# Kernel optimization log

Measured on AMD Instinct MI355X. Metric: run time of the kernel, lower is better.

Reference implementation:

```python
import jax, jax.numpy as jnp
import numpy as np
from jax import lax

STRIDE = 2
PADDING = 2
KERNEL = 5


def _conv_transpose3d(x, weight, bias):
    # weight: [C_in, C_out, kd, kh, kw] (PyTorch ConvTranspose3d layout)
    # Equivalent dense conv: flip kernel spatially, swap in/out channels,
    # lhs_dilation=stride, symmetric padding = dilation*(k-1) - padding.
    w_t = jnp.flip(weight, axis=(2, 3, 4)).transpose(1, 0, 2, 3, 4)  # [C_out, C_in, k,k,k]
    pad = KERNEL - 1 - PADDING  # = 2
    y = lax.conv_general_dilated(
        x, w_t,
        window_strides=(1, 1, 1),
        padding=[(pad, pad)] * 3,
        lhs_dilation=(STRIDE, STRIDE, STRIDE),
        dimension_numbers=("NCDHW", "OIDHW", "NCDHW"),
    )
    return y + bias[None, :, None, None, None]


def _maxpool3d(y, k):
    # PyTorch MaxPool3d(kernel=k) -> stride=k, no padding, floor mode == VALID
    win = (1, 1, k, k, k)
    return lax.reduce_window(y, -jnp.inf, lax.max, win, win, "VALID")


def setup_inputs() -> dict:
    key = jax.random.key(0)
    k1, k2, k3 = jax.random.split(key, 3)
    x = jax.random.normal(k1, (16, 32, 16, 32, 32), dtype=jnp.float32)
    weight = jax.random.normal(k2, (32, 64, 5, 5, 5), dtype=jnp.float32) * 0.05
    bias = jax.random.normal(k3, (64,), dtype=jnp.float32) * 0.05
    return {"x": x, "weight": weight, "bias": bias}


def reference(x, weight, bias):
    y = _conv_transpose3d(x, weight, bias)     # [16, 64, 31, 63, 63]
    y = _maxpool3d(y, 2)                       # [16, 64, 15, 31, 31]
    y = _maxpool3d(y, 3)                       # [16, 64, 5, 10, 10]
    return jnp.sum(y, axis=1, keepdims=True)   # [16, 1, 5, 10, 10]
```

## Files before the change

kernel.cpp:

```cpp
#include <hip/hip_runtime.h>
#include <hip/hip_bf16.h>
#include <math.h>

typedef short bf16x8 __attribute__((ext_vector_type(8)));
typedef float f32x4 __attribute__((ext_vector_type(4)));

constexpr int CIN = 32, COUT = 64, D = 16, H = 32, W = 32;

constexpr size_t WS_NEED = 884736u;

static __device__ const unsigned char IT_CODE[24] = {
    0, 8, 16, 3,
    1, 9, 17, 11, 19, 7,
    2, 10, 18, 5, 13, 21, 15,
    4, 12, 20, 6, 14, 22, 23};
static __device__ const unsigned char IT_START[5] = {0, 4, 10, 17, 24};
static __device__ const unsigned char EPI_START[10] = {0, 1, 3, 5, 6, 7, 9, 11, 12, 13};
static __device__ const unsigned char EPI_CNT[10]   = {1, 2, 2, 1, 1, 2, 2, 1, 1, 2};

__global__ void prep_w(const float* __restrict__ w, unsigned short* __restrict__ wtp) {
    int idx = blockIdx.x * 256 + threadIdx.x;
    int ci  = idx & 31;
    int co  = (idx >> 5) & 63;
    int tt  = idx >> 11;
    int t   = tt % 27, cls = tt / 27;
    int td = t / 9, th = (t / 3) % 3, tw = t % 3;
    int pd = (cls >> 2) & 1, ph = (cls >> 1) & 1, pw = cls & 1;
    int kd = pd + 2 * td, kh = ph + 2 * th, kw = pw + 2 * tw;
    float v = 0.f;
    if (kd < 5 && kh < 5 && kw < 5)
        v = w[(ci * COUT + co) * 125 + kd * 25 + kh * 5 + kw];
    __hip_bfloat16 b = __float2bfloat16(v);
    wtp[idx] = *reinterpret_cast<unsigned short*>(&b);
}

__device__ __forceinline__ int lpA(int wrow, int quad) {
    return wrow * 64 + ((quad ^ ((wrow >> 1) & 3)) << 4);
}

#define MFMA_G(nt, bb)                                                                       \
    acc[0][0][nt] = __builtin_amdgcn_mfma_f32_16x16x32_bf16(a##bb##0, b##bb##nt, acc[0][0][nt], 0, 0, 0); \
    acc[0][1][nt] = __builtin_amdgcn_mfma_f32_16x16x32_bf16(a##bb##1, b##bb##nt, acc[0][1][nt], 0, 0, 0); \
    acc[1][0][nt] = __builtin_amdgcn_mfma_f32_16x16x32_bf16(a##bb##2, b##bb##nt, acc[1][0][nt], 0, 0, 0); \
    acc[1][1][nt] = __builtin_amdgcn_mfma_f32_16x16x32_bf16(a##bb##3, b##bb##nt, acc[1][1][nt], 0, 0, 0); \
    acc[2][0][nt] = __builtin_amdgcn_mfma_f32_16x16x32_bf16(a##bb##4, b##bb##nt, acc[2][0][nt], 0, 0, 0); \
    acc[2][1][nt] = __builtin_amdgcn_mfma_f32_16x16x32_bf16(a##bb##5, b##bb##nt, acc[2][1][nt], 0, 0, 0);

#define LOADTAP(S)                                                                   \
    {                                                                                \
        int Boff = __builtin_amdgcn_readfirstlane((ptd * 9 + pth * 3 + ptw) * 4096); \
        int Qb   = __builtin_amdgcn_readfirstlane(((alpha + 2 - ptd) * 5 + (2 - pth)) * 2048); \
        int ss   = __builtin_amdgcn_readfirstlane(2 - ptw);                          \
        b##S##0 = *(const bf16x8*)(tbb + Boff);                                      \
        b##S##1 = *(const bf16x8*)(tbb + Boff + 1024);                               \
        b##S##2 = *(const bf16x8*)(tbb + Boff + 2048);                               \
        b##S##3 = *(const bf16x8*)(tbb + Boff + 3072);                               \
        int lpa = ss == 0 ? lp00 : (ss == 1 ? lp01 : lp02);                          \
        int lpb = ss == 0 ? lp10 : (ss == 1 ? lp11 : lp12);                          \
        const char* rb = xsb + Qb;                                                   \
        a##S##0 = *(const bf16x8*)(rb + lpa);                                        \
        a##S##1 = *(const bf16x8*)(rb + lpb);                                        \
        a##S##2 = *(const bf16x8*)(rb + 2048 + lpa);                                 \
        a##S##3 = *(const bf16x8*)(rb + 2048 + lpb);                                 \
        a##S##4 = *(const bf16x8*)(rb + 4096 + lpa);                                 \
        a##S##5 = *(const bf16x8*)(rb + 4096 + lpb);                                 \
    }

__global__ __launch_bounds__(256, 2) void main_k(
    const unsigned short* __restrict__ wtp, const float* __restrict__ x,
    const float* __restrict__ bias, float* __restrict__ out)
{
    __shared__ unsigned short Xs[25600];
    int bx = blockIdx.x;
    int h0 = bx % 10;
    int d0 = (bx / 10) % 5;
    int n  = bx / 50;
    int tid = threadIdx.x;

    int id0 = 3 * d0 - 1, ih0 = 3 * h0 - 1;
#pragma unroll 5
    for (int u = tid; u < 6400; u += 256) {
        int q  = u & 7;
        int ci = (u >> 3) & 31;
        int p  = u >> 8;
        int dd = p / 5, hl = p % 5;
        int id = id0 + dd, ih = ih0 + hl;
        float4 v = {0.f, 0.f, 0.f, 0.f};
        if (id >= 0 && ih >= 0)
            v = ((const float4*)(x + (((size_t)(n * CIN + ci) * D + id) * H + ih) * W))[q];
        unsigned short hj[4];
        {
            __hip_bfloat16 b0 = __float2bfloat16(v.x); hj[0] = *reinterpret_cast<unsigned short*>(&b0);
            __hip_bfloat16 b1 = __float2bfloat16(v.y); hj[1] = *reinterpret_cast<unsigned short*>(&b1);
            __hip_bfloat16 b2 = __float2bfloat16(v.z); hj[2] = *reinterpret_cast<unsigned short*>(&b2);
            __hip_bfloat16 b3 = __float2bfloat16(v.w); hj[3] = *reinterpret_cast<unsigned short*>(&b3);
        }
        int rowb = p * 1024;
        int cig = ci >> 3, cil = ci & 7;
#pragma unroll
        for (int j = 0; j < 4; ++j) {
            int ww = 4 * q + 1 + j;
            if (ww < 32)
                Xs[rowb + ww * 32 + ((cig ^ ((ww >> 1) & 3)) << 3) + cil] = hj[j];
        }
        if (q == 0)
            Xs[rowb + (cig << 3) + cil] = 0;
    }

    int lane = tid & 63, wv = tid >> 6;
    int l15 = lane & 15, quad = lane >> 4;
    int wv_s = __builtin_amdgcn_readfirstlane(wv);

    int laneB = l15 * 64 + quad * 16;
    int m1 = 16 + l15; if (m1 > 29) m1 = 29;
    int lp00 = lpA(l15 + 0, quad), lp01 = lpA(l15 + 1, quad), lp02 = lpA(l15 + 2, quad);
    int lp10 = lpA(m1 + 0, quad),  lp11 = lpA(m1 + 1, quad),  lp12 = lpA(m1 + 2, quad);

    int fsm0 = (0x3123 >> (quad * 4)) & 15;
    int fsm1 = (0x4312 >> (quad * 4)) & 15;

    float mxp[2][4][2];
#pragma unroll
    for (int mt = 0; mt < 2; ++mt)
#pragma unroll
        for (int nt = 0; nt < 4; ++nt) { mxp[mt][nt][0] = -INFINITY; mxp[mt][nt][1] = -INFINITY; }

    __syncthreads();
    const char* xsb = (const char*)Xs;

    int it0 = IT_START[wv_s], it1 = IT_START[wv_s + 1];
#pragma unroll 1
    for (int ii = it0; ii < it1; ++ii) {
        int code  = __builtin_amdgcn_readfirstlane(IT_CODE[ii]);
        int cls   = code & 7;
        int alpha = code >> 3;
        int ntd = 3 - ((cls >> 2) & 1), nth = 3 - ((cls >> 1) & 1), ntw = 3 - (cls & 1);
        const char* tbb = (const char*)wtp + (size_t)cls * 27 * 4096 + laneB;
        const int T = ntd * nth * ntw;

        f32x4 acc[3][2][4];
#pragma unroll
        for (int b = 0; b < 3; ++b)
#pragma unroll
            for (int mt = 0; mt < 2; ++mt)
#pragma unroll
                for (int nt = 0; nt < 4; ++nt) acc[b][mt][nt] = (f32x4){0.f, 0.f, 0.f, 0.f};

        int ptd = 0, pth = 0, ptw = 0, tl = 0;
        auto adv = [&]() {
            if (tl + 1 < T) {
                ++tl; ++ptw;
                if (ptw == ntw) { ptw = 0; ++pth; if (pth == nth) { pth = 0; ++ptd; } }
            }
        };

        bf16x8 bE0, bE1, bE2, bE3, aE0, aE1, aE2, aE3, aE4, aE5;
        bf16x8 bO0, bO1, bO2, bO3, aO0, aO1, aO2, aO3, aO4, aO5;
        LOADTAP(E) adv();
        LOADTAP(O) adv();

#pragma unroll 1
        for (int t = 0; t + 1 < T; t += 2) {
            __builtin_amdgcn_s_setprio(1);
            MFMA_G(0, E) MFMA_G(1, E) MFMA_G(2, E) MFMA_G(3, E)
            __builtin_amdgcn_s_setprio(0);
            LOADTAP(E) adv();
            __builtin_amdgcn_s_setprio(1);
            MFMA_G(0, O) MFMA_G(1, O) MFMA_G(2, O) MFMA_G(3, O)
            __builtin_amdgcn_s_setprio(0);
            LOADTAP(O) adv();
        }
        if (T & 1) {
            __builtin_amdgcn_s_setprio(1);
            MFMA_G(0, E) MFMA_G(1, E) MFMA_G(2, E) MFMA_G(3, E)
            __builtin_amdgcn_s_setprio(0);
        }

#pragma unroll
        for (int mt = 0; mt < 2; ++mt) {
            int fs = mt ? fsm1 : fsm0;
#pragma unroll
            for (int nt = 0; nt < 4; ++nt) {
                float r0 = fmaxf(fmaxf(acc[0][mt][nt][0], acc[1][mt][nt][0]), acc[2][mt][nt][0]);
                float r1 = fmaxf(fmaxf(acc[0][mt][nt][1], acc[1][mt][nt][1]), acc[2][mt][nt][1]);
                float r2 = fmaxf(fmaxf(acc[0][mt][nt][2], acc[1][mt][nt][2]), acc[2][mt][nt][2]);
                float r3 = fmaxf(fmaxf(acc[0][mt][nt][3], acc[1][mt][nt][3]), acc[2][mt][nt][3]);
                float t01 = fmaxf(r0, r1), t012 = fmaxf(t01, r2), t0123 = fmaxf(t012, r3);
                float pA = fs == 1 ? r0 : (fs == 2 ? t01 : (fs == 3 ? t012 : t0123));
                float t23 = fmaxf(r2, r3), t123 = fmaxf(r1, t23);
                float pB = fs == 1 ? t123 : (fs == 2 ? t23 : (fs == 3 ? r3 : -INFINITY));
                mxp[mt][nt][0] = fmaxf(mxp[mt][nt][0], pA);
                mxp[mt][nt][1] = fmaxf(mxp[mt][nt][1], pB);
            }
        }
    }

    __syncthreads();
    float* epi = (float*)Xs;
#pragma unroll
    for (int mt = 0; mt < 2; ++mt) {
        int g = mt * 4 + quad;
#pragma unroll
        for (int nt = 0; nt < 4; ++nt) {
            epi[((wv * 8 + g) * 2 + 0) * 64 + nt * 16 + l15] = mxp[mt][nt][0];
            epi[((wv * 8 + g) * 2 + 1) * 64 + nt * 16 + l15] = mxp[mt][nt][1];
        }
    }
    __syncthreads();

    int elemBase = ((n * 5 + d0) * 10 + h0) * 10;
    float bco = bias[lane];
#pragma unroll 1
    for (int win = wv_s; win < 10; win += 4) {
        int st = EPI_START[win], cnt = EPI_CNT[win];
        float v = -INFINITY;
        for (int src = 0; src < 4; ++src)
            for (int e = st; e < st + cnt; ++e)
                v = fmaxf(v, epi[(src * 16 + e) * 64 + lane]);
        v += bco;
#pragma unroll
        for (int off = 32; off > 0; off >>= 1) v += __shfl_xor(v, off);
        if (lane == 0) out[elemBase + win] = v;
    }
}

__global__ __launch_bounds__(256) void fused_fallback(
    const float* __restrict__ x, const float* __restrict__ wsrc,
    const float* __restrict__ bias, float* __restrict__ out)
{
    __shared__ float xs[CIN * 125];
    __shared__ float wmax[4][64];
    const int b  = blockIdx.x;
    const int w0 = b % 10, h0 = (b / 10) % 10, d0 = (b / 100) % 5, n = b / 500;
    const int tid = threadIdx.x;
    const int id0 = 3 * d0 - 1, ih0 = 3 * h0 - 1, iw0 = 3 * w0 - 1;
    for (int e = tid; e < CIN * 125; e += 256) {
        int kk = e % 5, jj = (e / 5) % 5, ii = (e / 25) % 5, c = e / 125;
        int id = id0 + ii, ih = ih0 + jj, iw = iw0 + kk;
        float v = 0.f;
        if (id >= 0 && ih >= 0 && iw >= 0)
            v = x[(((n * CIN + c) * D + id) * H + ih) * W + iw];
        xs[e] = v;
    }
    __syncthreads();
    const int lane = tid & 63, wv = tid >> 6;
    float lmax = -INFINITY;
    for (int ccls = 0; ccls < 2; ++ccls) {
        const int cls = wv * 2 + ccls;
        const int pd = (cls >> 2) & 1, ph = (cls >> 1) & 1, pw = cls & 1;
        float acc[27];
#pragma unroll
        for (int i = 0; i < 27; ++i) acc[i] = 0.f;
        for (int ci = 0; ci < CIN; ++ci) {
            float wr[27];
#pragma unroll
            for (int t = 0; t < 27; ++t) {
                int td = t / 9, th = (t / 3) % 3, tw = t % 3;
                int kd = pd + 2 * td, kh = ph + 2 * th, kw = pw + 2 * tw;
                wr[t] = (kd < 5 && kh < 5 && kw < 5)
                          ? wsrc[((ci * 64 + lane) * 125) + kd * 25 + kh * 5 + kw] : 0.f;
            }
            const float* xb = xs + ci * 125;
#pragma unroll
            for (int td = 0; td < 3; ++td)
#pragma unroll
            for (int th = 0; th < 3; ++th)
#pragma unroll
            for (int tw = 0; tw < 3; ++tw) {
                const float wval = wr[(td * 3 + th) * 3 + tw];
#pragma unroll
                for (int a = 0; a < 3; ++a)
#pragma unroll
                for (int bb = 0; bb < 3; ++bb)
#pragma unroll
                for (int cc = 0; cc < 3; ++cc)
                    acc[(a * 3 + bb) * 3 + cc] +=
                        xb[(a + 2 - td) * 25 + (bb + 2 - th) * 5 + (cc + 2 - tw)] * wval;
            }
        }
#pragma unroll
        for (int i = 0; i < 27; ++i) lmax = fmaxf(lmax, acc[i]);
    }
    wmax[wv][lane] = lmax;
    __syncthreads();
    if (wv == 0) {
        float m = fmaxf(fmaxf(wmax[0][lane], wmax[1][lane]),
                        fmaxf(wmax[2][lane], wmax[3][lane]));
        m += bias[lane];
        for (int off = 32; off > 0; off >>= 1) m += __shfl_down(m, off);
        if (lane == 0) out[b] = m;
    }
}

extern "C" void kernel_launch(void* const* d_in, const int* in_sizes, int n_in,
                              void* d_out, int out_size, void* d_ws, size_t ws_size,
                              hipStream_t stream) {
    const float* x    = (const float*)d_in[0];
    const float* w    = (const float*)d_in[1];
    const float* bias = (const float*)d_in[2];
    float* out = (float*)d_out;

    if (ws_size >= WS_NEED) {
        unsigned short* wtp = (unsigned short*)d_ws;
        prep_w<<<1728, 256, 0, stream>>>(w, wtp);
        main_k<<<800, 256, 0, stream>>>(wtp, x, bias, out);
    } else {
        fused_fallback<<<8000, 256, 0, stream>>>(x, w, bias, out);
    }
}
```

Baseline: 205.2 us.

## Switch main conv GEMM from 16x16x32 to 32x32x16 MFMA tiles

Replaces the 16x16x32 bf16 MFMA tiling with 32x32x16 MFMA, so each wave accumulates six 32x32 output tiles per tap. A and B operand addressing and the pooling fold are rewritten to match the new accumulator lane layout, and the epilogue scatters partial maxima into per-window LDS slots that are reduced with a fixed 8-way max. The aim is fewer MFMA instructions and LDS operand loads per FLOP, at the cost of more accumulator registers and a different epilogue shape. The tap loop also drops the clamped advance and guards the prefetches directly.

```diff
diff --git a/kernel.cpp b/kernel.cpp
--- a/kernel.cpp
+++ b/kernel.cpp
@@ -3,7 +3,7 @@
 #include <math.h>
 
 typedef short bf16x8 __attribute__((ext_vector_type(8)));
-typedef float f32x4 __attribute__((ext_vector_type(4)));
+typedef float f32x16 __attribute__((ext_vector_type(16)));
 
 constexpr int CIN = 32, COUT = 64, D = 16, H = 32, W = 32;
 
@@ -15,8 +15,6 @@
     2, 10, 18, 5, 13, 21, 15,
     4, 12, 20, 6, 14, 22, 23};
 static __device__ const unsigned char IT_START[5] = {0, 4, 10, 17, 24};
-static __device__ const unsigned char EPI_START[10] = {0, 1, 3, 5, 6, 7, 9, 11, 12, 13};
-static __device__ const unsigned char EPI_CNT[10]   = {1, 2, 2, 1, 1, 2, 2, 1, 1, 2};
 
 __global__ void prep_w(const float* __restrict__ w, unsigned short* __restrict__ wtp) {
     int idx = blockIdx.x * 256 + threadIdx.x;
@@ -34,36 +32,70 @@
     wtp[idx] = *reinterpret_cast<unsigned short*>(&b);
 }
 
-__device__ __forceinline__ int lpA(int wrow, int quad) {
-    return wrow * 64 + ((quad ^ ((wrow >> 1) & 3)) << 4);
-}
-
-#define MFMA_G(nt, bb)                                                                       \
-    acc[0][0][nt] = __builtin_amdgcn_mfma_f32_16x16x32_bf16(a##bb##0, b##bb##nt, acc[0][0][nt], 0, 0, 0); \
-    acc[0][1][nt] = __builtin_amdgcn_mfma_f32_16x16x32_bf16(a##bb##1, b##bb##nt, acc[0][1][nt], 0, 0, 0); \
-    acc[1][0][nt] = __builtin_amdgcn_mfma_f32_16x16x32_bf16(a##bb##2, b##bb##nt, acc[1][0][nt], 0, 0, 0); \
-    acc[1][1][nt] = __builtin_amdgcn_mfma_f32_16x16x32_bf16(a##bb##3, b##bb##nt, acc[1][1][nt], 0, 0, 0); \
-    acc[2][0][nt] = __builtin_amdgcn_mfma_f32_16x16x32_bf16(a##bb##4, b##bb##nt, acc[2][0][nt], 0, 0, 0); \
-    acc[2][1][nt] = __builtin_amdgcn_mfma_f32_16x16x32_bf16(a##bb##5, b##bb##nt, acc[2][1][nt], 0, 0, 0);
+__device__ __forceinline__ int lpA32(int row, int g) {
+    return row * 64 + ((g ^ ((row >> 1) & 3)) << 4);
+}
+
+#define RFL(x) __builtin_amdgcn_readfirstlane(x)
 
 #define LOADTAP(S)                                                                   \
     {                                                                                \
-        int Boff = __builtin_amdgcn_readfirstlane((ptd * 9 + pth * 3 + ptw) * 4096); \
-        int Qb   = __builtin_amdgcn_readfirstlane(((alpha + 2 - ptd) * 5 + (2 - pth)) * 2048); \
-        int ss   = __builtin_amdgcn_readfirstlane(2 - ptw);                          \
-        b##S##0 = *(const bf16x8*)(tbb + Boff);                                      \
-        b##S##1 = *(const bf16x8*)(tbb + Boff + 1024);                               \
-        b##S##2 = *(const bf16x8*)(tbb + Boff + 2048);                               \
-        b##S##3 = *(const bf16x8*)(tbb + Boff + 3072);                               \
-        int lpa = ss == 0 ? lp00 : (ss == 1 ? lp01 : lp02);                          \
-        int lpb = ss == 0 ? lp10 : (ss == 1 ? lp11 : lp12);                          \
+        int Boff = RFL((ptd * 9 + pth * 3 + ptw) * 4096);                            \
+        int Qb   = RFL(((alpha + 2 - ptd) * 5 + (2 - pth)) * 2048);                  \
+        int ss   = RFL(2 - ptw);                                                     \
+        const char* bq = tbb + Boff;                                                 \
+        b##S##00 = *(const bf16x8*)(bq);                                             \
+        b##S##01 = *(const bf16x8*)(bq + 32);                                        \
+        b##S##10 = *(const bf16x8*)(bq + 2048);                                      \
+        b##S##11 = *(const bf16x8*)(bq + 2048 + 32);                                 \
+        int la0 = ss == 0 ? lpx00 : (ss == 1 ? lpx10 : lpx20);                       \
+        int la1 = ss == 0 ? lpx01 : (ss == 1 ? lpx11 : lpx21);                       \
         const char* rb = xsb + Qb;                                                   \
-        a##S##0 = *(const bf16x8*)(rb + lpa);                                        \
-        a##S##1 = *(const bf16x8*)(rb + lpb);                                        \
-        a##S##2 = *(const bf16x8*)(rb + 2048 + lpa);                                 \
-        a##S##3 = *(const bf16x8*)(rb + 2048 + lpb);                                 \
-        a##S##4 = *(const bf16x8*)(rb + 4096 + lpa);                                 \
-        a##S##5 = *(const bf16x8*)(rb + 4096 + lpb);                                 \
+        a##S##00 = *(const bf16x8*)(rb + la0);                                       \
+        a##S##01 = *(const bf16x8*)(rb + la1);                                       \
+        a##S##10 = *(const bf16x8*)(rb + 2048 + la0);                                \
+        a##S##11 = *(const bf16x8*)(rb + 2048 + la1);                                \
+        a##S##20 = *(const bf16x8*)(rb + 4096 + la0);                                \
+        a##S##21 = *(const bf16x8*)(rb + 4096 + la1);                                \
+    }
+
+#define BURST(S)                                                                     \
+    __builtin_amdgcn_s_setprio(1);                                                   \
+    c00 = __builtin_amdgcn_mfma_f32_32x32x16_bf16(a##S##00, b##S##00, c00, 0, 0, 0); \
+    c01 = __builtin_amdgcn_mfma_f32_32x32x16_bf16(a##S##00, b##S##10, c01, 0, 0, 0); \
+    c10 = __builtin_amdgcn_mfma_f32_32x32x16_bf16(a##S##10, b##S##00, c10, 0, 0, 0); \
+    c11 = __builtin_amdgcn_mfma_f32_32x32x16_bf16(a##S##10, b##S##10, c11, 0, 0, 0); \
+    c20 = __builtin_amdgcn_mfma_f32_32x32x16_bf16(a##S##20, b##S##00, c20, 0, 0, 0); \
+    c21 = __builtin_amdgcn_mfma_f32_32x32x16_bf16(a##S##20, b##S##10, c21, 0, 0, 0); \
+    c00 = __builtin_amdgcn_mfma_f32_32x32x16_bf16(a##S##01, b##S##01, c00, 0, 0, 0); \
+    c01 = __builtin_amdgcn_mfma_f32_32x32x16_bf16(a##S##01, b##S##11, c01, 0, 0, 0); \
+    c10 = __builtin_amdgcn_mfma_f32_32x32x16_bf16(a##S##11, b##S##01, c10, 0, 0, 0); \
+    c11 = __builtin_amdgcn_mfma_f32_32x32x16_bf16(a##S##11, b##S##11, c11, 0, 0, 0); \
+    c20 = __builtin_amdgcn_mfma_f32_32x32x16_bf16(a##S##21, b##S##01, c20, 0, 0, 0); \
+    c21 = __builtin_amdgcn_mfma_f32_32x32x16_bf16(a##S##21, b##S##11, c21, 0, 0, 0); \
+    __builtin_amdgcn_s_setprio(0);
+
+#define FOLDNT(NT, A0, A1, A2)                                                       \
+    {                                                                                \
+        float r[16];                                                                 \
+        _Pragma("unroll")                                                            \
+        for (int i = 0; i < 16; ++i) r[i] = fmaxf(fmaxf(A0[i], A1[i]), A2[i]);       \
+        float s0 = half ? fmaxf(r[0], r[1]) : fmaxf(fmaxf(r[0], r[1]), r[2]);        \
+        float s1 = half ? fmaxf(r[2], r[3]) : r[3];                                  \
+        float s2 = half ? fmaxf(fmaxf(r[4], r[5]), r[6]) : r[4];                     \
+        float s3 = half ? r[7] : fmaxf(fmaxf(r[5], r[6]), r[7]);                     \
+        float s4 = half ? r[8] : fmaxf(r[8], r[9]);                                  \
+        float s5 = half ? fmaxf(fmaxf(r[9], r[10]), r[11]) : fmaxf(r[10], r[11]);    \
+        float s6 = half ? fmaxf(r[12], r[13]) : fmaxf(fmaxf(r[12], r[13]), r[14]);   \
+        float s7 = half ? -INFINITY : r[15];                                         \
+        mxp[NT][0] = fmaxf(mxp[NT][0], s0);                                          \
+        mxp[NT][1] = fmaxf(mxp[NT][1], s1);                                          \
+        mxp[NT][2] = fmaxf(mxp[NT][2], s2);                                          \
+        mxp[NT][3] = fmaxf(mxp[NT][3], s3);                                          \
+        mxp[NT][4] = fmaxf(mxp[NT][4], s4);                                          \
+        mxp[NT][5] = fmaxf(mxp[NT][5], s5);                                          \
+        mxp[NT][6] = fmaxf(mxp[NT][6], s6);                                          \
+        mxp[NT][7] = fmaxf(mxp[NT][7], s7);                                          \
     }
 
 __global__ __launch_bounds__(256, 2) void main_k(
@@ -108,22 +140,21 @@
     }
 
     int lane = tid & 63, wv = tid >> 6;
-    int l15 = lane & 15, quad = lane >> 4;
+    int l31 = lane & 31, half = lane >> 5;
     int wv_s = __builtin_amdgcn_readfirstlane(wv);
 
-    int laneB = l15 * 64 + quad * 16;
-    int m1 = 16 + l15; if (m1 > 29) m1 = 29;
-    int lp00 = lpA(l15 + 0, quad), lp01 = lpA(l15 + 1, quad), lp02 = lpA(l15 + 2, quad);
-    int lp10 = lpA(m1 + 0, quad),  lp11 = lpA(m1 + 1, quad),  lp12 = lpA(m1 + 2, quad);
-
-    int fsm0 = (0x3123 >> (quad * 4)) & 15;
-    int fsm1 = (0x4312 >> (quad * 4)) & 15;
-
-    float mxp[2][4][2];
-#pragma unroll
-    for (int mt = 0; mt < 2; ++mt)
-#pragma unroll
-        for (int nt = 0; nt < 4; ++nt) { mxp[mt][nt][0] = -INFINITY; mxp[mt][nt][1] = -INFINITY; }
+    int laneB32 = l31 * 64 + (half << 4);
+
+    int r0c = l31, r1c = l31 + 1 > 31 ? 31 : l31 + 1, r2c = l31 + 2 > 31 ? 31 : l31 + 2;
+    int lpx00 = lpA32(r0c, half),     lpx01 = lpA32(r0c, half + 2);
+    int lpx10 = lpA32(r1c, half),     lpx11 = lpA32(r1c, half + 2);
+    int lpx20 = lpA32(r2c, half),     lpx21 = lpA32(r2c, half + 2);
+
+    float mxp[2][8];
+#pragma unroll
+    for (int nt = 0; nt < 2; ++nt)
+#pragma unroll
+        for (int s = 0; s < 8; ++s) mxp[nt][s] = -INFINITY;
 
     __syncthreads();
     const char* xsb = (const char*)Xs;
@@ -131,79 +162,55 @@
     int it0 = IT_START[wv_s], it1 = IT_START[wv_s + 1];
 #pragma unroll 1
     for (int ii = it0; ii < it1; ++ii) {
-        int code  = __builtin_amdgcn_readfirstlane(IT_CODE[ii]);
+        int code  = RFL(IT_CODE[ii]);
         int cls   = code & 7;
         int alpha = code >> 3;
         int ntd = 3 - ((cls >> 2) & 1), nth = 3 - ((cls >> 1) & 1), ntw = 3 - (cls & 1);
-        const char* tbb = (const char*)wtp + (size_t)cls * 27 * 4096 + laneB;
+        const char* tbb = (const char*)wtp + (size_t)cls * 27 * 4096 + laneB32;
         const int T = ntd * nth * ntw;
 
-        f32x4 acc[3][2][4];
-#pragma unroll
-        for (int b = 0; b < 3; ++b)
-#pragma unroll
-            for (int mt = 0; mt < 2; ++mt)
-#pragma unroll
-                for (int nt = 0; nt < 4; ++nt) acc[b][mt][nt] = (f32x4){0.f, 0.f, 0.f, 0.f};
-
-        int ptd = 0, pth = 0, ptw = 0, tl = 0;
+        f32x16 c00 = {}, c01 = {}, c10 = {}, c11 = {}, c20 = {}, c21 = {};
+
+        int ptd = 0, pth = 0, ptw = 0;
         auto adv = [&]() {
-            if (tl + 1 < T) {
-                ++tl; ++ptw;
-                if (ptw == ntw) { ptw = 0; ++pth; if (pth == nth) { pth = 0; ++ptd; } }
-            }
+            ++ptw;
+            if (ptw == ntw) { ptw = 0; ++pth; if (pth == nth) { pth = 0; ++ptd; } }
         };
 
-        bf16x8 bE0, bE1, bE2, bE3, aE0, aE1, aE2, aE3, aE4, aE5;
-        bf16x8 bO0, bO1, bO2, bO3, aO0, aO1, aO2, aO3, aO4, aO5;
+        bf16x8 aE00, aE01, aE10, aE11, aE20, aE21, bE00, bE01, bE10, bE11;
+        bf16x8 aO00, aO01, aO10, aO11, aO20, aO21, bO00, bO01, bO10, bO11;
         LOADTAP(E) adv();
         LOADTAP(O) adv();
 
 #pragma unroll 1
-        for (int t = 0; t + 1 < T; t += 2) {
-            __builtin_amdgcn_s_setprio(1);
-            MFMA_G(0, E) MFMA_G(1, E) MFMA_G(2, E) MFMA_G(3, E)
-            __builtin_amdgcn_s_setprio(0);
-            LOADTAP(E) adv();
-            __builtin_amdgcn_s_setprio(1);
-            MFMA_G(0, O) MFMA_G(1, O) MFMA_G(2, O) MFMA_G(3, O)
-            __builtin_amdgcn_s_setprio(0);
-            LOADTAP(O) adv();
-        }
-        if (T & 1) {
-            __builtin_amdgcn_s_setprio(1);
-            MFMA_G(0, E) MFMA_G(1, E) MFMA_G(2, E) MFMA_G(3, E)
-            __builtin_amdgcn_s_setprio(0);
-        }
-
-#pragma unroll
-        for (int mt = 0; mt < 2; ++mt) {
-            int fs = mt ? fsm1 : fsm0;
-#pragma unroll
-            for (int nt = 0; nt < 4; ++nt) {
-                float r0 = fmaxf(fmaxf(acc[0][mt][nt][0], acc[1][mt][nt][0]), acc[2][mt][nt][0]);
-                float r1 = fmaxf(fmaxf(acc[0][mt][nt][1], acc[1][mt][nt][1]), acc[2][mt][nt][1]);
-                float r2 = fmaxf(fmaxf(acc[0][mt][nt][2], acc[1][mt][nt][2]), acc[2][mt][nt][2]);
-                float r3 = fmaxf(fmaxf(acc[0][mt][nt][3], acc[1][mt][nt][3]), acc[2][mt][nt][3]);
-                float t01 = fmaxf(r0, r1), t012 = fmaxf(t01, r2), t0123 = fmaxf(t012, r3);
-                float pA = fs == 1 ? r0 : (fs == 2 ? t01 : (fs == 3 ? t012 : t0123));
-                float t23 = fmaxf(r2, r3), t123 = fmaxf(r1, t23);
-                float pB = fs == 1 ? t123 : (fs == 2 ? t23 : (fs == 3 ? r3 : -INFINITY));
-                mxp[mt][nt][0] = fmaxf(mxp[mt][nt][0], pA);
-                mxp[mt][nt][1] = fmaxf(mxp[mt][nt][1], pB);
+        for (int t = 0; t < T; t += 2) {
+            BURST(E)
+            if (t + 2 < T) { LOADTAP(E) adv(); }
+            if (t + 1 < T) {
+                BURST(O)
+                if (t + 3 < T) { LOADTAP(O) adv(); }
             }
         }
+
+        FOLDNT(0, c00, c10, c20)
+        FOLDNT(1, c01, c11, c21)
     }
 
     __syncthreads();
     float* epi = (float*)Xs;
-#pragma unroll
-    for (int mt = 0; mt < 2; ++mt) {
-        int g = mt * 4 + quad;
-#pragma unroll
-        for (int nt = 0; nt < 4; ++nt) {
-            epi[((wv * 8 + g) * 2 + 0) * 64 + nt * 16 + l15] = mxp[mt][nt][0];
-            epi[((wv * 8 + g) * 2 + 1) * 64 + nt * 16 + l15] = mxp[mt][nt][1];
+    for (int u = tid; u < 5120; u += 256) epi[u] = -INFINITY;
+    __syncthreads();
+    {
+        int src = wv * 2 + half;
+        const int w0tab[8] = {0, 1, 2, 3, 5, 6, 8, 9};
+        const int w1tab[8] = {1, 2, 4, 5, 6, 7, 9, 9};
+#pragma unroll
+        for (int s = 0; s < 8; ++s) {
+            int wn = half ? w1tab[s] : w0tab[s];
+            if (!half || s < 7) {
+                epi[(wn * 8 + src) * 64 + l31]      = mxp[0][s];
+                epi[(wn * 8 + src) * 64 + 32 + l31] = mxp[1][s];
+            }
         }
     }
     __syncthreads();
@@ -212,11 +219,9 @@
     float bco = bias[lane];
 #pragma unroll 1
     for (int win = wv_s; win < 10; win += 4) {
-        int st = EPI_START[win], cnt = EPI_CNT[win];
         float v = -INFINITY;
-        for (int src = 0; src < 4; ++src)
-            for (int e = st; e < st + cnt; ++e)
-                v = fmaxf(v, epi[(src * 16 + e) * 64 + lane]);
+#pragma unroll
+        for (int s = 0; s < 8; ++s) v = fmaxf(v, epi[(win * 8 + s) * 64 + lane]);
         v += bco;
 #pragma unroll
         for (int off = 32; off > 0; off >>= 1) v += __shfl_xor(v, off);
```

Result: slower. 212.5 us (+3.5%).

## Split output channels across wave pairs with 512-thread blocks and decoupled A/B prefetch

Applied to the files above, without the earlier changes.

Doubles the block to 512 threads so that two waves share each iteration list, each computing half of the 64 output channels. This halves per-wave accumulators and B registers and allows more resident waves (launch bounds 512,4). The A and B operand prefetch is restructured so a single A buffer is reloaded between bursts while B uses double buffering. In exchange, each A tile is now loaded from LDS by two waves, adding LDS traffic, and the tail handling for odd tap counts changes.

```diff
diff --git a/kernel.cpp b/kernel.cpp
--- a/kernel.cpp
+++ b/kernel.cpp
@@ -38,35 +38,51 @@
     return wrow * 64 + ((quad ^ ((wrow >> 1) & 3)) << 4);
 }
 
-#define MFMA_G(nt, bb)                                                                       \
-    acc[0][0][nt] = __builtin_amdgcn_mfma_f32_16x16x32_bf16(a##bb##0, b##bb##nt, acc[0][0][nt], 0, 0, 0); \
-    acc[0][1][nt] = __builtin_amdgcn_mfma_f32_16x16x32_bf16(a##bb##1, b##bb##nt, acc[0][1][nt], 0, 0, 0); \
-    acc[1][0][nt] = __builtin_amdgcn_mfma_f32_16x16x32_bf16(a##bb##2, b##bb##nt, acc[1][0][nt], 0, 0, 0); \
-    acc[1][1][nt] = __builtin_amdgcn_mfma_f32_16x16x32_bf16(a##bb##3, b##bb##nt, acc[1][1][nt], 0, 0, 0); \
-    acc[2][0][nt] = __builtin_amdgcn_mfma_f32_16x16x32_bf16(a##bb##4, b##bb##nt, acc[2][0][nt], 0, 0, 0); \
-    acc[2][1][nt] = __builtin_amdgcn_mfma_f32_16x16x32_bf16(a##bb##5, b##bb##nt, acc[2][1][nt], 0, 0, 0);
-
-#define LOADTAP(S)                                                                   \
+#define RFL(x) __builtin_amdgcn_readfirstlane(x)
+
+#define BURST(bp)                                                                          \
+    __builtin_amdgcn_s_setprio(1);                                                         \
+    acc[0][0][0] = __builtin_amdgcn_mfma_f32_16x16x32_bf16(aa0, bp##0, acc[0][0][0], 0, 0, 0); \
+    acc[0][1][0] = __builtin_amdgcn_mfma_f32_16x16x32_bf16(aa1, bp##0, acc[0][1][0], 0, 0, 0); \
+    acc[1][0][0] = __builtin_amdgcn_mfma_f32_16x16x32_bf16(aa2, bp##0, acc[1][0][0], 0, 0, 0); \
+    acc[1][1][0] = __builtin_amdgcn_mfma_f32_16x16x32_bf16(aa3, bp##0, acc[1][1][0], 0, 0, 0); \
+    acc[2][0][0] = __builtin_amdgcn_mfma_f32_16x16x32_bf16(aa4, bp##0, acc[2][0][0], 0, 0, 0); \
+    acc[2][1][0] = __builtin_amdgcn_mfma_f32_16x16x32_bf16(aa5, bp##0, acc[2][1][0], 0, 0, 0); \
+    acc[0][0][1] = __builtin_amdgcn_mfma_f32_16x16x32_bf16(aa0, bp##1, acc[0][0][1], 0, 0, 0); \
+    acc[0][1][1] = __builtin_amdgcn_mfma_f32_16x16x32_bf16(aa1, bp##1, acc[0][1][1], 0, 0, 0); \
+    acc[1][0][1] = __builtin_amdgcn_mfma_f32_16x16x32_bf16(aa2, bp##1, acc[1][0][1], 0, 0, 0); \
+    acc[1][1][1] = __builtin_amdgcn_mfma_f32_16x16x32_bf16(aa3, bp##1, acc[1][1][1], 0, 0, 0); \
+    acc[2][0][1] = __builtin_amdgcn_mfma_f32_16x16x32_bf16(aa4, bp##1, acc[2][0][1], 0, 0, 0); \
+    acc[2][1][1] = __builtin_amdgcn_mfma_f32_16x16x32_bf16(aa5, bp##1, acc[2][1][1], 0, 0, 0); \
+    __builtin_amdgcn_s_setprio(0);
+
+#define LOADA()                                                                      \
     {                                                                                \
-        int Boff = __builtin_amdgcn_readfirstlane((ptd * 9 + pth * 3 + ptw) * 4096); \
-        int Qb   = __builtin_amdgcn_readfirstlane(((alpha + 2 - ptd) * 5 + (2 - pth)) * 2048); \
-        int ss   = __builtin_amdgcn_readfirstlane(2 - ptw);                          \
+        int Qb = RFL(((alpha + 2 - aptd) * 5 + (2 - apth)) * 2048);                  \
+        int ss = RFL(2 - aptw);                                                      \
+        int la = ss == 0 ? lp00 : (ss == 1 ? lp01 : lp02);                           \
+        int lb = ss == 0 ? lp10 : (ss == 1 ? lp11 : lp12);                           \
+        const char* rb = xsb + Qb;                                                   \
+        aa0 = *(const bf16x8*)(rb + la);                                             \
+        aa1 = *(const bf16x8*)(rb + lb);                                             \
+        aa2 = *(const bf16x8*)(rb + 2048 + la);                                      \
+        aa3 = *(const bf16x8*)(rb + 2048 + lb);                                      \
+        aa4 = *(const bf16x8*)(rb + 4096 + la);                                      \
+        aa5 = *(const bf16x8*)(rb + 4096 + lb);                                      \
+    }
+#define ADVA()                                                                       \
+    { ++aptw; if (aptw == ntw) { aptw = 0; ++apth; if (apth == nth) { apth = 0; ++aptd; } } }
+
+#define LOADB(S)                                                                     \
+    {                                                                                \
+        int Boff = RFL((bptd * 9 + bpth * 3 + bptw) * 4096);                         \
         b##S##0 = *(const bf16x8*)(tbb + Boff);                                      \
         b##S##1 = *(const bf16x8*)(tbb + Boff + 1024);                               \
-        b##S##2 = *(const bf16x8*)(tbb + Boff + 2048);                               \
-        b##S##3 = *(const bf16x8*)(tbb + Boff + 3072);                               \
-        int lpa = ss == 0 ? lp00 : (ss == 1 ? lp01 : lp02);                          \
-        int lpb = ss == 0 ? lp10 : (ss == 1 ? lp11 : lp12);                          \
-        const char* rb = xsb + Qb;                                                   \
-        a##S##0 = *(const bf16x8*)(rb + lpa);                                        \
-        a##S##1 = *(const bf16x8*)(rb + lpb);                                        \
-        a##S##2 = *(const bf16x8*)(rb + 2048 + lpa);                                 \
-        a##S##3 = *(const bf16x8*)(rb + 2048 + lpb);                                 \
-        a##S##4 = *(const bf16x8*)(rb + 4096 + lpa);                                 \
-        a##S##5 = *(const bf16x8*)(rb + 4096 + lpb);                                 \
-    }
-
-__global__ __launch_bounds__(256, 2) void main_k(
+    }
+#define ADVB()                                                                       \
+    { ++bptw; if (bptw == ntw) { bptw = 0; ++bpth; if (bpth == nth) { bpth = 0; ++bptd; } } }
+
+__global__ __launch_bounds__(512, 4) void main_k(
     const unsigned short* __restrict__ wtp, const float* __restrict__ x,
     const float* __restrict__ bias, float* __restrict__ out)
 {
@@ -78,8 +94,8 @@
     int tid = threadIdx.x;
 
     int id0 = 3 * d0 - 1, ih0 = 3 * h0 - 1;
-#pragma unroll 5
-    for (int u = tid; u < 6400; u += 256) {
+#pragma unroll 4
+    for (int u = tid; u < 6400; u += 512) {
         int q  = u & 7;
         int ci = (u >> 3) & 31;
         int p  = u >> 8;
@@ -109,7 +125,8 @@
 
     int lane = tid & 63, wv = tid >> 6;
     int l15 = lane & 15, quad = lane >> 4;
-    int wv_s = __builtin_amdgcn_readfirstlane(wv);
+    int wl  = RFL(wv >> 1);
+    int coh = RFL(wv & 1);
 
     int laneB = l15 * 64 + quad * 16;
     int m1 = 16 + l15; if (m1 > 29) m1 = 29;
@@ -119,68 +136,60 @@
     int fsm0 = (0x3123 >> (quad * 4)) & 15;
     int fsm1 = (0x4312 >> (quad * 4)) & 15;
 
-    float mxp[2][4][2];
+    float mxp[2][2][2];
 #pragma unroll
     for (int mt = 0; mt < 2; ++mt)
 #pragma unroll
-        for (int nt = 0; nt < 4; ++nt) { mxp[mt][nt][0] = -INFINITY; mxp[mt][nt][1] = -INFINITY; }
+        for (int nt = 0; nt < 2; ++nt) { mxp[mt][nt][0] = -INFINITY; mxp[mt][nt][1] = -INFINITY; }
 
     __syncthreads();
     const char* xsb = (const char*)Xs;
 
-    int it0 = IT_START[wv_s], it1 = IT_START[wv_s + 1];
+    int it0 = IT_START[wl], it1 = IT_START[wl + 1];
 #pragma unroll 1
     for (int ii = it0; ii < it1; ++ii) {
-        int code  = __builtin_amdgcn_readfirstlane(IT_CODE[ii]);
+        int code  = RFL(IT_CODE[ii]);
         int cls   = code & 7;
         int alpha = code >> 3;
         int ntd = 3 - ((cls >> 2) & 1), nth = 3 - ((cls >> 1) & 1), ntw = 3 - (cls & 1);
-        const char* tbb = (const char*)wtp + (size_t)cls * 27 * 4096 + laneB;
+        const char* tbb = (const char*)wtp + (size_t)cls * 27 * 4096 + coh * 2048 + laneB;
         const int T = ntd * nth * ntw;
 
-        f32x4 acc[3][2][4];
+        f32x4 acc[3][2][2];
 #pragma unroll
         for (int b = 0; b < 3; ++b)
 #pragma unroll
             for (int mt = 0; mt < 2; ++mt)
 #pragma unroll
-                for (int nt = 0; nt < 4; ++nt) acc[b][mt][nt] = (f32x4){0.f, 0.f, 0.f, 0.f};
-
-        int ptd = 0, pth = 0, ptw = 0, tl = 0;
-        auto adv = [&]() {
-            if (tl + 1 < T) {
-                ++tl; ++ptw;
-                if (ptw == ntw) { ptw = 0; ++pth; if (pth == nth) { pth = 0; ++ptd; } }
+                for (int nt = 0; nt < 2; ++nt) acc[b][mt][nt] = (f32x4){0.f, 0.f, 0.f, 0.f};
+
+        int aptd = 0, apth = 0, aptw = 0;
+        int bptd = 0, bpth = 0, bptw = 0;
+
+        bf16x8 aa0, aa1, aa2, aa3, aa4, aa5;
+        bf16x8 bE0, bE1, bO0, bO1;
+
+        LOADB(E) ADVB()
+        LOADB(O) ADVB()
+        LOADA()
+
+#pragma unroll 1
+        for (int t = 0; t < T; t += 2) {
+            BURST(bE)
+            if (t + 1 < T) { ADVA() LOADA() }
+            if (t + 2 < T) { LOADB(E) ADVB() }
+            if (t + 1 < T) {
+                BURST(bO)
+                if (t + 2 < T) { ADVA() LOADA() }
+                if (t + 3 < T) { LOADB(O) ADVB() }
             }
-        };
-
-        bf16x8 bE0, bE1, bE2, bE3, aE0, aE1, aE2, aE3, aE4, aE5;
-        bf16x8 bO0, bO1, bO2, bO3, aO0, aO1, aO2, aO3, aO4, aO5;
-        LOADTAP(E) adv();
-        LOADTAP(O) adv();
-
-#pragma unroll 1
-        for (int t = 0; t + 1 < T; t += 2) {
-            __builtin_amdgcn_s_setprio(1);
-            MFMA_G(0, E) MFMA_G(1, E) MFMA_G(2, E) MFMA_G(3, E)
-            __builtin_amdgcn_s_setprio(0);
-            LOADTAP(E) adv();
-            __builtin_amdgcn_s_setprio(1);
-            MFMA_G(0, O) MFMA_G(1, O) MFMA_G(2, O) MFMA_G(3, O)
-            __builtin_amdgcn_s_setprio(0);
-            LOADTAP(O) adv();
-        }
-        if (T & 1) {
-            __builtin_amdgcn_s_setprio(1);
-            MFMA_G(0, E) MFMA_G(1, E) MFMA_G(2, E) MFMA_G(3, E)
-            __builtin_amdgcn_s_setprio(0);
         }
 
 #pragma unroll
         for (int mt = 0; mt < 2; ++mt) {
             int fs = mt ? fsm1 : fsm0;
 #pragma unroll
-            for (int nt = 0; nt < 4; ++nt) {
+            for (int nt = 0; nt < 2; ++nt) {
                 float r0 = fmaxf(fmaxf(acc[0][mt][nt][0], acc[1][mt][nt][0]), acc[2][mt][nt][0]);
                 float r1 = fmaxf(fmaxf(acc[0][mt][nt][1], acc[1][mt][nt][1]), acc[2][mt][nt][1]);
                 float r2 = fmaxf(fmaxf(acc[0][mt][nt][2], acc[1][mt][nt][2]), acc[2][mt][nt][2]);
@@ -201,17 +210,19 @@
     for (int mt = 0; mt < 2; ++mt) {
         int g = mt * 4 + quad;
 #pragma unroll
-        for (int nt = 0; nt < 4; ++nt) {
-            epi[((wv * 8 + g) * 2 + 0) * 64 + nt * 16 + l15] = mxp[mt][nt][0];
-            epi[((wv * 8 + g) * 2 + 1) * 64 + nt * 16 + l15] = mxp[mt][nt][1];
+        for (int nt = 0; nt < 2; ++nt) {
+            int co = coh * 32 + nt * 16 + l15;
+            epi[((wl * 8 + g) * 2 + 0) * 64 + co] = mxp[mt][nt][0];
+            epi[((wl * 8 + g) * 2 + 1) * 64 + co] = mxp[mt][nt][1];
         }
     }
     __syncthreads();
 
     int elemBase = ((n * 5 + d0) * 10 + h0) * 10;
     float bco = bias[lane];
+    int wv_s = RFL(wv);
 #pragma unroll 1
-    for (int win = wv_s; win < 10; win += 4) {
+    for (int win = wv_s; win < 10; win += 8) {
         int st = EPI_START[win], cnt = EPI_CNT[win];
         float v = -INFINITY;
         for (int src = 0; src < 4; ++src)
@@ -303,7 +314,7 @@
     if (ws_size >= WS_NEED) {
         unsigned short* wtp = (unsigned short*)d_ws;
         prep_w<<<1728, 256, 0, stream>>>(w, wtp);
-        main_k<<<800, 256, 0, stream>>>(wtp, x, bias, out);
+        main_k<<<800, 512, 0, stream>>>(wtp, x, bias, out);
     } else {
         fused_fallback<<<8000, 256, 0, stream>>>(x, w, bias, out);
     }
```

Measured after the change: 197.4 us. 3.8% less time.
